# Kernel tuning notes

Hardware: AMD Instinct MI355X
Metric: run time of the kernel (lower is better)

The kernel has to match this reference:

```python
import jax, jax.numpy as jnp
import numpy as np
import math

B, S, H, N = 64, 512, 768, 16
C_COMP, C_REL = 5, 3
P = N * (N - 1)
LN_EPS = 1e-5

# ordered pair indices (i, j), i != j, row-major like the torch double loop
_PAIR_I, _PAIR_J = np.nonzero(~np.eye(N, dtype=bool))
_PAIR_I = jnp.asarray(_PAIR_I)
_PAIR_J = jnp.asarray(_PAIR_J)


def setup_inputs() -> dict:
    key = jax.random.key(0)
    ks = jax.random.split(key, 20)
    sc = 0.02
    p = lambda k, shape: (jax.random.normal(k, shape, jnp.float32) * sc)
    return {
        "last_hidden_state": jax.random.normal(ks[0], (B, S, H), jnp.float32),
        "span_starts": jax.random.randint(ks[1], (B, N), 0, 480).astype(jnp.int32),
        "span_lengths": jax.random.randint(ks[2], (B, N), 0, 31).astype(jnp.int32),
        "components": jax.random.randint(ks[3], (B, N), 0, C_COMP).astype(jnp.int32),
        "relations": jax.random.randint(ks[4], (B, P), 0, C_REL).astype(jnp.int32),
        # comp_classifier: Linear(H,512) -> Tanh -> Linear(512,C_COMP)
        "comp_w1": p(ks[5], (H, 512)), "comp_b1": jnp.zeros((512,), jnp.float32),
        "comp_w2": p(ks[6], (512, C_COMP)), "comp_b2": jnp.zeros((C_COMP,), jnp.float32),
        # Attention(H, H), no bias
        "wq": p(ks[7], (H, H)), "wk": p(ks[8], (H, H)), "wv": p(ks[9], (H, H)),
        # LayerNorm(H)
        "ln_g": jnp.ones((H,), jnp.float32), "ln_b": jnp.zeros((H,), jnp.float32),
        # rel_classifier: Linear(2H,512) -> Tanh -> Linear(512,C_REL)
        "rel_w1": p(ks[10], (2 * H, 512)), "rel_b1": jnp.zeros((512,), jnp.float32),
        "rel_w2": p(ks[11], (512, C_REL)), "rel_b2": jnp.zeros((C_REL,), jnp.float32),
    }


def _ce_mean(logits, gold):
    # logits [M, C], gold [M] -> scalar mean cross entropy
    logp = jax.nn.log_softmax(logits, axis=-1)
    return -jnp.mean(jnp.take_along_axis(logp, gold[:, None].astype(jnp.int32), axis=-1))


def reference(last_hidden_state, span_starts, span_lengths, components, relations,
              comp_w1, comp_b1, comp_w2, comp_b2,
              wq, wk, wv, ln_g, ln_b,
              rel_w1, rel_b1, rel_w2, rel_b2):
    # --- per-span mean pooling (inclusive end = start + length), masked+vectorized ---
    pos = jnp.arange(S)
    ends = span_starts + span_lengths
    mask = ((pos[None, None, :] >= span_starts[:, :, None]) &
            (pos[None, None, :] <= ends[:, :, None])).astype(jnp.float32)  # [B,N,S]
    lens = (span_lengths + 1).astype(jnp.float32)
    pooled = jnp.einsum('bns,bsh->bnh', mask, last_hidden_state) / lens[:, :, None]  # [B,N,H]
    # dropout(p=0.2) is identity in eval mode

    # --- component classifier ---
    comp_logits = jnp.tanh(pooled @ comp_w1 + comp_b1) @ comp_w2 + comp_b2  # [B,N,C_COMP]

    # --- small self-attention over spans ---
    q = pooled @ wq; k = pooled @ wk; v = pooled @ wv
    scores = jax.nn.softmax(jnp.einsum('bnd,bmd->bnm', q, k) / math.sqrt(H), axis=-1)
    attn = jnp.einsum('bnm,bmh->bnh', scores, v)

    # --- residual + layernorm ---
    x = pooled + attn
    mu = jnp.mean(x, axis=-1, keepdims=True)
    var = jnp.mean((x - mu) ** 2, axis=-1, keepdims=True)
    x = (x - mu) * jax.lax.rsqrt(var + LN_EPS) * ln_g + ln_b  # [B,N,H]

    # --- O(N^2) pairwise relation classification (ordered pairs i != j) ---
    pair_feat = jnp.concatenate([x[:, _PAIR_I, :], x[:, _PAIR_J, :]], axis=-1)  # [B,P,2H]
    rel_logits = jnp.tanh(pair_feat @ rel_w1 + rel_b1) @ rel_w2 + rel_b2  # [B,P,C_REL]

    loss_comp = _ce_mean(comp_logits.reshape(-1, C_COMP), components.reshape(-1))
    loss_rel = _ce_mean(rel_logits.reshape(-1, C_REL), relations.reshape(-1))
    return (comp_logits.reshape(-1, C_COMP), rel_logits.reshape(-1, C_REL), loss_comp, loss_rel)
```

## Files before the change

kernel.cpp:

```cpp
#include <hip/hip_runtime.h>

#define BB 64
#define SS 512
#define HH 768
#define NSPAN 16
#define PP 240
#define CCOMP 5
#define CREL 3

typedef unsigned short u16;
typedef __attribute__((ext_vector_type(8))) short bf16x8;
typedef __attribute__((ext_vector_type(4))) float f32x4;

__device__ __forceinline__ u16 f2bf(float f) {
    union { float f; unsigned int i; } v; v.f = f;
    unsigned int x = v.i;
    unsigned int lsb = (x >> 16) & 1u;
    x += 0x7fffu + lsb;
    return (u16)(x >> 16);
}

__device__ __forceinline__ float ftanh(float x) {
    float xc = fminf(fmaxf(x, -15.f), 15.f);
    float e = __expf(2.f * xc);
    return (e - 1.f) / (e + 1.f);
}

__global__ __launch_bounds__(256) void prep_pool_kernel(
    const float* __restrict__ cw1, const float* __restrict__ wq,
    const float* __restrict__ wk, const float* __restrict__ wv,
    const float* __restrict__ rw1, u16* __restrict__ wcat_t, u16* __restrict__ relw_t,
    const float* __restrict__ lhs, const int* __restrict__ starts,
    const int* __restrict__ lens, float* __restrict__ pooled, u16* __restrict__ pooled_bf) {
    __shared__ u16 Ls[32][36];
    int tid = threadIdx.x;
    if (blockIdx.x < 2880) {
        int blk = blockIdx.x;
        const float* W; int ldw, nt; u16* outp;
        if (blk < 384)        {             W = cw1; ldw = 512; nt = 16; outp = wcat_t; }
        else if (blk < 960)   { blk -= 384; W = wq;  ldw = 768; nt = 24; outp = wcat_t + (size_t)512 * 768; }
        else if (blk < 1536)  { blk -= 960; W = wk;  ldw = 768; nt = 24; outp = wcat_t + (size_t)1280 * 768; }
        else if (blk < 2112)  { blk -= 1536; W = wv; ldw = 768; nt = 24; outp = wcat_t + (size_t)2048 * 768; }
        else if (blk < 2496)  { blk -= 2112; W = rw1; ldw = 512; nt = 16; outp = relw_t; }
        else                  { blk -= 2496; W = rw1 + (size_t)768 * 512; ldw = 512; nt = 16; outp = relw_t + (size_t)512 * 768; }
        int tk = blk / nt, tn = blk % nt;
        int k0 = tk * 32, n0 = tn * 32;
        int tx = tid & 31, ty = tid >> 5;
#pragma unroll
        for (int r = 0; r < 4; ++r) {
            int k = ty + r * 8;
            Ls[tx][k] = f2bf(W[(size_t)(k0 + k) * ldw + n0 + tx]);
        }
        __syncthreads();
#pragma unroll
        for (int r = 0; r < 4; ++r) {
            int n = ty + r * 8;
            outp[(size_t)(n0 + n) * 768 + k0 + tx] = Ls[n][tx];
        }
    } else {
        int bn = blockIdx.x - 2880;
        int b = bn >> 4;
        int st = starts[bn];
        int ln = lens[bn];
        const float* base = lhs + ((size_t)b * SS + st) * HH;
        float a0 = 0.f, a1 = 0.f, a2 = 0.f;
        for (int s = 0; s <= ln; ++s) {
            const float* row = base + (size_t)s * HH;
            a0 += row[tid];
            a1 += row[tid + 256];
            a2 += row[tid + 512];
        }
        float inv = 1.0f / (float)(ln + 1);
        a0 *= inv; a1 *= inv; a2 *= inv;
        float* out = pooled + (size_t)bn * HH;
        u16* outb = pooled_bf + (size_t)bn * HH;
        out[tid] = a0;       out[tid + 256] = a1;       out[tid + 512] = a2;
        outb[tid] = f2bf(a0); outb[tid + 256] = f2bf(a1); outb[tid + 512] = f2bf(a2);
    }
}

__global__ __launch_bounds__(256) void gemm_pw_kernel(
    const u16* __restrict__ pooled_bf, const u16* __restrict__ wcat_t,
    const float* __restrict__ comp_b1, float* __restrict__ y2) {
    __shared__ u16 As[128][72];
    __shared__ u16 Bs[64][72];
    int ccol0 = blockIdx.x * 64;
    int row0 = blockIdx.y * 128;
    int act = (ccol0 < 512);
    int tid = threadIdx.x;
    int lane = tid & 63, w = tid >> 6;
    int q = lane >> 4, l15 = lane & 15;
    int wm = w * 32;
    int r = tid >> 2, c0 = (tid & 3) * 16;
    const u16* ga = pooled_bf + (size_t)(row0 + r) * 768 + c0;
    const u16* gb = wcat_t + (size_t)(ccol0 + r) * 768 + c0;
    const u16* ga2 = ga + (size_t)64 * 768;
    f32x4 acc[2][4];
#pragma unroll
    for (int i = 0; i < 2; ++i)
#pragma unroll
        for (int j = 0; j < 4; ++j) acc[i][j] = (f32x4){0.f, 0.f, 0.f, 0.f};

    uint4 va00 = *(const uint4*)(ga);
    uint4 va01 = *(const uint4*)(ga + 8);
    uint4 va10 = *(const uint4*)(ga2);
    uint4 va11 = *(const uint4*)(ga2 + 8);
    uint4 vb0 = *(const uint4*)(gb);
    uint4 vb1 = *(const uint4*)(gb + 8);
    for (int k0 = 0; k0 < 768; k0 += 64) {
        __syncthreads();
        *(uint4*)(&As[r][c0]) = va00;
        *(uint4*)(&As[r][c0 + 8]) = va01;
        *(uint4*)(&As[r + 64][c0]) = va10;
        *(uint4*)(&As[r + 64][c0 + 8]) = va11;
        *(uint4*)(&Bs[r][c0]) = vb0;
        *(uint4*)(&Bs[r][c0 + 8]) = vb1;
        __syncthreads();
        if (k0 + 64 < 768) {
            va00 = *(const uint4*)(ga + k0 + 64);
            va01 = *(const uint4*)(ga + k0 + 72);
            va10 = *(const uint4*)(ga2 + k0 + 64);
            va11 = *(const uint4*)(ga2 + k0 + 72);
            vb0 = *(const uint4*)(gb + k0 + 64);
            vb1 = *(const uint4*)(gb + k0 + 72);
        }
#pragma unroll
        for (int ks = 0; ks < 2; ++ks) {
            bf16x8 a0 = *(const bf16x8*)(&As[wm + l15][ks * 32 + q * 8]);
            bf16x8 a1 = *(const bf16x8*)(&As[wm + 16 + l15][ks * 32 + q * 8]);
#pragma unroll
            for (int tn = 0; tn < 4; ++tn) {
                bf16x8 bt = *(const bf16x8*)(&Bs[tn * 16 + l15][ks * 32 + q * 8]);
                acc[0][tn] = __builtin_amdgcn_mfma_f32_16x16x32_bf16(a0, bt, acc[0][tn], 0, 0, 0);
                acc[1][tn] = __builtin_amdgcn_mfma_f32_16x16x32_bf16(a1, bt, acc[1][tn], 0, 0, 0);
            }
        }
    }
#pragma unroll
    for (int tm = 0; tm < 2; ++tm)
#pragma unroll
        for (int tn = 0; tn < 4; ++tn)
#pragma unroll
            for (int reg = 0; reg < 4; ++reg) {
                int rr = row0 + wm + tm * 16 + q * 4 + reg;
                int cc = ccol0 + tn * 16 + l15;
                float v = acc[tm][tn][reg];
                if (act) v = ftanh(v + comp_b1[cc]);
                y2[(size_t)rr * 2816 + cc] = v;
            }
}

__global__ __launch_bounds__(256) void gemm_z_kernel(
    const u16* __restrict__ x_bf, const u16* __restrict__ relw_t, float* __restrict__ Z) {
    __shared__ u16 As[32][72];
    __shared__ u16 Bs[64][72];
    int ccol0 = blockIdx.x * 64;
    int row0 = blockIdx.y * 32;
    int tid = threadIdx.x;
    int lane = tid & 63, w = tid >> 6;
    int q = lane >> 4, l15 = lane & 15;
    int wm = (w & 1) * 16, wn = (w >> 1) * 32;
    int ra = tid >> 3, ca = (tid & 7) * 8;
    int rb = tid >> 2, cb = (tid & 3) * 16;
    const u16* ga = x_bf + (size_t)(row0 + ra) * 768 + ca;
    const u16* gb = relw_t + (size_t)(ccol0 + rb) * 768 + cb;
    f32x4 acc[2];
    acc[0] = (f32x4){0.f, 0.f, 0.f, 0.f};
    acc[1] = (f32x4){0.f, 0.f, 0.f, 0.f};

    uint4 va = *(const uint4*)(ga);
    uint4 vb0 = *(const uint4*)(gb);
    uint4 vb1 = *(const uint4*)(gb + 8);
    for (int k0 = 0; k0 < 768; k0 += 64) {
        __syncthreads();
        *(uint4*)(&As[ra][ca]) = va;
        *(uint4*)(&Bs[rb][cb]) = vb0;
        *(uint4*)(&Bs[rb][cb + 8]) = vb1;
        __syncthreads();
        if (k0 + 64 < 768) {
            va = *(const uint4*)(ga + k0 + 64);
            vb0 = *(const uint4*)(gb + k0 + 64);
            vb1 = *(const uint4*)(gb + k0 + 72);
        }
#pragma unroll
        for (int ks = 0; ks < 2; ++ks) {
            bf16x8 a0 = *(const bf16x8*)(&As[wm + l15][ks * 32 + q * 8]);
            bf16x8 b0 = *(const bf16x8*)(&Bs[wn + l15][ks * 32 + q * 8]);
            bf16x8 b1 = *(const bf16x8*)(&Bs[wn + 16 + l15][ks * 32 + q * 8]);
            acc[0] = __builtin_amdgcn_mfma_f32_16x16x32_bf16(a0, b0, acc[0], 0, 0, 0);
            acc[1] = __builtin_amdgcn_mfma_f32_16x16x32_bf16(a0, b1, acc[1], 0, 0, 0);
        }
    }
#pragma unroll
    for (int tn = 0; tn < 2; ++tn)
#pragma unroll
        for (int reg = 0; reg < 4; ++reg) {
            int rr = row0 + wm + q * 4 + reg;
            int cc = ccol0 + wn + tn * 16 + l15;
            Z[(size_t)rr * 1024 + cc] = acc[tn][reg];
        }
}

__global__ __launch_bounds__(256) void attn_ln_kernel(
    const float* __restrict__ y2, const float* __restrict__ pooled,
    const float* __restrict__ ln_g, const float* __restrict__ ln_b,
    u16* __restrict__ x_bf) {
    __shared__ float ks[16][772];
    __shared__ float Ssm[16][17];
    int b = blockIdx.x;
    int tid = threadIdx.x;
    int n = tid >> 4;
    int hl = tid & 15;

    for (int u = 0; u < 48; ++u) {
        int h = hl + (u << 4);
        ks[n][h] = y2[((size_t)(b * 16 + n)) * 2816 + 1280 + h];
    }
    __syncthreads();

    int m = tid & 15;
    const float* qrow = y2 + ((size_t)(b * 16 + n)) * 2816 + 512;
    float dot = 0.f;
    for (int h = 0; h < 768; h += 4) {
        float4 qv = *(const float4*)(qrow + h);
        float4 kv = *(const float4*)(&ks[m][h]);
        dot += qv.x * kv.x + qv.y * kv.y + qv.z * kv.z + qv.w * kv.w;
    }
    float sval = dot * 0.03608439182435161f;
    float mx = sval;
#pragma unroll
    for (int off = 8; off >= 1; off >>= 1) mx = fmaxf(mx, __shfl_xor(mx, off, 16));
    float pexp = __expf(sval - mx);
    float psum = pexp;
#pragma unroll
    for (int off = 8; off >= 1; off >>= 1) psum += __shfl_xor(psum, off, 16);
    Ssm[n][m] = pexp / psum;
    __syncthreads();

    for (int u = 0; u < 48; ++u) {
        int h = hl + (u << 4);
        ks[n][h] = y2[((size_t)(b * 16 + n)) * 2816 + 2048 + h];
    }
    __syncthreads();

    float sc[16];
#pragma unroll
    for (int mm = 0; mm < 16; ++mm) sc[mm] = Ssm[n][mm];
    int row = b * 16 + n;
    const float* prow = pooled + (size_t)row * HH;
    float xv[48];
    float ssum = 0.f, ssq = 0.f;
    for (int u = 0; u < 48; ++u) {
        int h = hl + (u << 4);
        float a = 0.f;
#pragma unroll
        for (int mm = 0; mm < 16; ++mm) a += sc[mm] * ks[mm][h];
        float v = prow[h] + a;
        xv[u] = v;
        ssum += v;
        ssq += v * v;
    }
#pragma unroll
    for (int off = 8; off >= 1; off >>= 1) {
        ssum += __shfl_xor(ssum, off, 16);
        ssq += __shfl_xor(ssq, off, 16);
    }
    float mu = ssum * (1.0f / 768.0f);
    float var = ssq * (1.0f / 768.0f) - mu * mu;
    float rs = rsqrtf(var + 1e-5f);
    u16* xrow_bf = x_bf + (size_t)row * HH;
    for (int u = 0; u < 48; ++u) {
        int h = hl + (u << 4);
        xrow_bf[h] = f2bf((xv[u] - mu) * rs * ln_g[h] + ln_b[h]);
    }
}

__global__ __launch_bounds__(256) void heads_kernel(
    const float* __restrict__ Z, const float* __restrict__ rb1,
    const float* __restrict__ rw2, const float* __restrict__ rb2,
    const int* __restrict__ rels,
    const float* __restrict__ y2, const float* __restrict__ cw2,
    const float* __restrict__ cb2, const int* __restrict__ comps,
    float* __restrict__ out, float* __restrict__ rel_p, float* __restrict__ comp_p) {
    __shared__ float Zs[16][1024];
    __shared__ float rw2s[1536];
    __shared__ float rb1s[512];
    __shared__ float red[4];
    int tid = threadIdx.x;
    int wave = tid >> 6, lane = tid & 63;
    if (blockIdx.x < 256) {
        int b = blockIdx.x >> 2;
        int quarter = blockIdx.x & 3;
        const float* zb = Z + (size_t)(b * 16) * 1024;
#pragma unroll
        for (int u = 0; u < 16; ++u) {
            *(float4*)(&Zs[u][tid * 4]) = *(const float4*)(zb + (size_t)u * 1024 + tid * 4);
        }
#pragma unroll
        for (int u = 0; u < 6; ++u) rw2s[tid + u * 256] = rw2[tid + u * 256];
        rb1s[tid] = rb1[tid];
        rb1s[tid + 256] = rb1[tid + 256];
        __syncthreads();

        float lsum = 0.f;
        for (int it = 0; it < 15; ++it) {
            int p = quarter * 60 + wave * 15 + it;
            int i = p / 15;
            int jj = p - i * 15;
            int j = jj + (jj >= i ? 1 : 0);
            float a0 = 0.f, a1 = 0.f, a2 = 0.f;
#pragma unroll
            for (int t = 0; t < 8; ++t) {
                int c = lane + (t << 6);
                float h = ftanh(Zs[i][c] + Zs[j][512 + c] + rb1s[c]);
                a0 += h * rw2s[c * 3 + 0];
                a1 += h * rw2s[c * 3 + 1];
                a2 += h * rw2s[c * 3 + 2];
            }
#pragma unroll
            for (int off = 32; off >= 1; off >>= 1) {
                a0 += __shfl_down(a0, off);
                a1 += __shfl_down(a1, off);
                a2 += __shfl_down(a2, off);
            }
            if (lane == 0) {
                int row = b * PP + p;
                float l0 = a0 + rb2[0];
                float l1 = a1 + rb2[1];
                float l2 = a2 + rb2[2];
                float mx = fmaxf(l0, fmaxf(l1, l2));
                float se = __expf(l0 - mx) + __expf(l1 - mx) + __expf(l2 - mx);
                float lse = __logf(se) + mx;
                int g = rels[row];
                float lg = (g == 0) ? l0 : ((g == 1) ? l1 : l2);
                lsum += lse - lg;
                float* o = out + 5120 + (size_t)row * 3;
                o[0] = l0; o[1] = l1; o[2] = l2;
            }
        }
        if (lane == 0) red[wave] = lsum;
        __syncthreads();
        if (tid == 0) rel_p[blockIdx.x] = red[0] + red[1] + red[2] + red[3];
    } else {
        int row = (blockIdx.x - 256) * 4 + wave;
        const float* hrow = y2 + (size_t)row * 2816;
        float acc[CCOMP] = {0.f, 0.f, 0.f, 0.f, 0.f};
#pragma unroll
        for (int t = 0; t < 8; ++t) {
            int c = lane + (t << 6);
            float h = hrow[c];
#pragma unroll
            for (int cc = 0; cc < CCOMP; ++cc) acc[cc] += h * cw2[c * CCOMP + cc];
        }
#pragma unroll
        for (int cc = 0; cc < CCOMP; ++cc)
#pragma unroll
            for (int off = 32; off >= 1; off >>= 1) acc[cc] += __shfl_down(acc[cc], off);
        if (lane == 0) {
            float l[CCOMP];
            float mx = -1e30f;
#pragma unroll
            for (int cc = 0; cc < CCOMP; ++cc) { l[cc] = acc[cc] + cb2[cc]; mx = fmaxf(mx, l[cc]); }
            float se = 0.f;
#pragma unroll
            for (int cc = 0; cc < CCOMP; ++cc) se += __expf(l[cc] - mx);
            float lse = __logf(se) + mx;
            red[wave] = lse - l[comps[row]];
#pragma unroll
            for (int cc = 0; cc < CCOMP; ++cc) out[row * CCOMP + cc] = l[cc];
        }
        __syncthreads();
        if (tid == 0) comp_p[blockIdx.x - 256] = red[0] + red[1] + red[2] + red[3];
    }
}

__global__ __launch_bounds__(256) void finalize_kernel(
    const float* __restrict__ comp_p, const float* __restrict__ rel_p,
    float* __restrict__ out) {
    __shared__ float rc[4], rr[4];
    int tid = threadIdx.x;
    int wave = tid >> 6, lane = tid & 63;
    float sc = comp_p[tid];
    float sr = rel_p[tid];
#pragma unroll
    for (int off = 32; off >= 1; off >>= 1) {
        sc += __shfl_down(sc, off);
        sr += __shfl_down(sr, off);
    }
    if (lane == 0) { rc[wave] = sc; rr[wave] = sr; }
    __syncthreads();
    if (tid == 0) {
        out[51200] = (rc[0] + rc[1] + rc[2] + rc[3]) * (1.0f / 1024.0f);
        out[51201] = (rr[0] + rr[1] + rr[2] + rr[3]) * (1.0f / 15360.0f);
    }
}

extern "C" void kernel_launch(void* const* d_in, const int* in_sizes, int n_in,
                              void* d_out, int out_size, void* d_ws, size_t ws_size,
                              hipStream_t stream) {
    const float* lhs     = (const float*)d_in[0];
    const int* starts    = (const int*)d_in[1];
    const int* lens      = (const int*)d_in[2];
    const int* comps     = (const int*)d_in[3];
    const int* rels      = (const int*)d_in[4];
    const float* comp_w1 = (const float*)d_in[5];
    const float* comp_b1 = (const float*)d_in[6];
    const float* comp_w2 = (const float*)d_in[7];
    const float* comp_b2 = (const float*)d_in[8];
    const float* wq      = (const float*)d_in[9];
    const float* wk      = (const float*)d_in[10];
    const float* wv      = (const float*)d_in[11];
    const float* ln_g    = (const float*)d_in[12];
    const float* ln_b    = (const float*)d_in[13];
    const float* rel_w1  = (const float*)d_in[14];
    const float* rel_b1  = (const float*)d_in[15];
    const float* rel_w2  = (const float*)d_in[16];
    const float* rel_b2  = (const float*)d_in[17];
    float* out = (float*)d_out;
    float* ws = (float*)d_ws;

    float* pooled = ws;
    float* y2     = pooled + 786432;
    float* Z      = y2 + 2883584;
    float* comp_p = Z + 1048576;
    float* rel_p  = comp_p + 256;
    u16* pooled_bf = (u16*)(rel_p + 256);
    u16* x_bf      = pooled_bf + 786432;
    u16* wcat_t    = x_bf + 786432;
    u16* relw_t    = wcat_t + 2162688;

    prep_pool_kernel<<<3904, 256, 0, stream>>>(comp_w1, wq, wk, wv, rel_w1, wcat_t, relw_t,
                                               lhs, starts, lens, pooled, pooled_bf);
    gemm_pw_kernel<<<dim3(44, 8), 256, 0, stream>>>(pooled_bf, wcat_t, comp_b1, y2);
    attn_ln_kernel<<<64, 256, 0, stream>>>(y2, pooled, ln_g, ln_b, x_bf);
    gemm_z_kernel<<<dim3(16, 32), 256, 0, stream>>>(x_bf, relw_t, Z);
    heads_kernel<<<512, 256, 0, stream>>>(Z, rel_b1, rel_w2, rel_b2, rels,
                                          y2, comp_w2, comp_b2, comps,
                                          out, rel_p, comp_p);
    finalize_kernel<<<1, 256, 0, stream>>>(comp_p, rel_p, out);
}
```

Baseline: 248.4 us.

## Fuse pipeline into single cooperative persistent kernel with grid syncs

Replaces six separate kernel launches with one cooperative kernel of 256 persistent blocks that loop over each stage's work units and use grid-wide syncs between stages. It keeps a multi-launch fallback selected by a phase argument if cooperative launch fails. The relation-head stage now stores Z in shared memory as bf16 instead of fp32. The intent is to remove launch gaps and inter-kernel drain, at the cost of lower per-stage parallelism, reduced occupancy from the large shared buffer, and grid-sync overhead.

```diff
diff --git a/kernel.cpp b/kernel.cpp
--- a/kernel.cpp
+++ b/kernel.cpp
@@ -1,9 +1,11 @@
 #include <hip/hip_runtime.h>
+#include <hip/hip_cooperative_groups.h>
+
+namespace cg = cooperative_groups;
 
 #define BB 64
 #define SS 512
 #define HH 768
-#define NSPAN 16
 #define PP 240
 #define CCOMP 5
 #define CREL 3
@@ -19,292 +21,333 @@
     x += 0x7fffu + lsb;
     return (u16)(x >> 16);
 }
-
+__device__ __forceinline__ float bf2f(u16 u) {
+    union { unsigned int i; float f; } v; v.i = ((unsigned int)u) << 16; return v.f;
+}
 __device__ __forceinline__ float ftanh(float x) {
     float xc = fminf(fmaxf(x, -15.f), 15.f);
     float e = __expf(2.f * xc);
     return (e - 1.f) / (e + 1.f);
 }
 
-__global__ __launch_bounds__(256) void prep_pool_kernel(
-    const float* __restrict__ cw1, const float* __restrict__ wq,
-    const float* __restrict__ wk, const float* __restrict__ wv,
-    const float* __restrict__ rw1, u16* __restrict__ wcat_t, u16* __restrict__ relw_t,
-    const float* __restrict__ lhs, const int* __restrict__ starts,
-    const int* __restrict__ lens, float* __restrict__ pooled, u16* __restrict__ pooled_bf) {
-    __shared__ u16 Ls[32][36];
-    int tid = threadIdx.x;
-    if (blockIdx.x < 2880) {
-        int blk = blockIdx.x;
-        const float* W; int ldw, nt; u16* outp;
-        if (blk < 384)        {             W = cw1; ldw = 512; nt = 16; outp = wcat_t; }
-        else if (blk < 960)   { blk -= 384; W = wq;  ldw = 768; nt = 24; outp = wcat_t + (size_t)512 * 768; }
-        else if (blk < 1536)  { blk -= 960; W = wk;  ldw = 768; nt = 24; outp = wcat_t + (size_t)1280 * 768; }
-        else if (blk < 2112)  { blk -= 1536; W = wv; ldw = 768; nt = 24; outp = wcat_t + (size_t)2048 * 768; }
-        else if (blk < 2496)  { blk -= 2112; W = rw1; ldw = 512; nt = 16; outp = relw_t; }
-        else                  { blk -= 2496; W = rw1 + (size_t)768 * 512; ldw = 512; nt = 16; outp = relw_t + (size_t)512 * 768; }
-        int tk = blk / nt, tn = blk % nt;
-        int k0 = tk * 32, n0 = tn * 32;
-        int tx = tid & 31, ty = tid >> 5;
-#pragma unroll
-        for (int r = 0; r < 4; ++r) {
-            int k = ty + r * 8;
-            Ls[tx][k] = f2bf(W[(size_t)(k0 + k) * ldw + n0 + tx]);
-        }
+__global__ __launch_bounds__(256) void fused_kernel(
+    const float* __restrict__ lhs, const int* __restrict__ starts, const int* __restrict__ lens,
+    const int* __restrict__ comps, const int* __restrict__ rels,
+    const float* __restrict__ cw1, const float* __restrict__ cb1,
+    const float* __restrict__ cw2, const float* __restrict__ cb2,
+    const float* __restrict__ wq, const float* __restrict__ wk, const float* __restrict__ wv,
+    const float* __restrict__ ln_g, const float* __restrict__ ln_b,
+    const float* __restrict__ rw1, const float* __restrict__ rb1,
+    const float* __restrict__ rw2, const float* __restrict__ rb2,
+    float* __restrict__ out, float* __restrict__ pooled, float* __restrict__ y2,
+    float* __restrict__ Z, float* __restrict__ comp_p, float* __restrict__ rel_p,
+    u16* __restrict__ pooled_bf, u16* __restrict__ x_bf,
+    u16* __restrict__ wcat_t, u16* __restrict__ relw_t, int phase) {
+    __shared__ __align__(16) char smem[50560];
+    const int tid = threadIdx.x;
+    const int blk = blockIdx.x;
+    const int gsz = (int)gridDim.x;
+    const int lane = tid & 63;
+    const int wid = tid >> 6;
+
+    if (phase == 0 || phase == 1) {
+        u16 (*Ls)[36] = (u16(*)[36])smem;
+        for (int u = blk; u < 3904; u += gsz) {
+            if (u < 2880) {
+                int b2 = u;
+                const float* W; int ldw, nt; u16* outp;
+                if (b2 < 384)        {             W = cw1; ldw = 512; nt = 16; outp = wcat_t; }
+                else if (b2 < 960)   { b2 -= 384;  W = wq;  ldw = 768; nt = 24; outp = wcat_t + (size_t)512 * 768; }
+                else if (b2 < 1536)  { b2 -= 960;  W = wk;  ldw = 768; nt = 24; outp = wcat_t + (size_t)1280 * 768; }
+                else if (b2 < 2112)  { b2 -= 1536; W = wv;  ldw = 768; nt = 24; outp = wcat_t + (size_t)2048 * 768; }
+                else if (b2 < 2496)  { b2 -= 2112; W = rw1; ldw = 512; nt = 16; outp = relw_t; }
+                else                 { b2 -= 2496; W = rw1 + (size_t)768 * 512; ldw = 512; nt = 16; outp = relw_t + (size_t)512 * 768; }
+                int tk = b2 / nt, tn = b2 % nt;
+                int k0 = tk * 32, n0 = tn * 32;
+                int tx = tid & 31, ty = tid >> 5;
+                __syncthreads();
+#pragma unroll
+                for (int r = 0; r < 4; ++r) {
+                    int k = ty + r * 8;
+                    Ls[tx][k] = f2bf(W[(size_t)(k0 + k) * ldw + n0 + tx]);
+                }
+                __syncthreads();
+#pragma unroll
+                for (int r = 0; r < 4; ++r) {
+                    int n = ty + r * 8;
+                    outp[(size_t)(n0 + n) * 768 + k0 + tx] = Ls[n][tx];
+                }
+            } else {
+                int bn = u - 2880;
+                int b = bn >> 4;
+                int st = starts[bn];
+                int ln = lens[bn];
+                const float* base = lhs + ((size_t)b * SS + st) * HH;
+                float a0 = 0.f, a1 = 0.f, a2 = 0.f;
+                for (int s = 0; s <= ln; ++s) {
+                    const float* row = base + (size_t)s * HH;
+                    a0 += row[tid];
+                    a1 += row[tid + 256];
+                    a2 += row[tid + 512];
+                }
+                float inv = 1.0f / (float)(ln + 1);
+                a0 *= inv; a1 *= inv; a2 *= inv;
+                float* o = pooled + (size_t)bn * HH;
+                u16* ob = pooled_bf + (size_t)bn * HH;
+                o[tid] = a0;        o[tid + 256] = a1;        o[tid + 512] = a2;
+                ob[tid] = f2bf(a0); ob[tid + 256] = f2bf(a1); ob[tid + 512] = f2bf(a2);
+            }
+        }
+    }
+    if (phase == 0) cg::this_grid().sync();
+
+    if (phase == 0 || phase == 2) {
+        u16 (*As)[72] = (u16(*)[72])smem;
+        u16 (*Bs)[72] = (u16(*)[72])(smem + 18432);
+        for (int t = blk; t < 352; t += gsz) {
+            int ccol0 = (t % 44) * 64;
+            int row0 = (t / 44) * 128;
+            int act = (ccol0 < 512);
+            int q = lane >> 4, l15 = lane & 15;
+            int wm = wid * 32;
+            int r = tid >> 2, c0 = (tid & 3) * 16;
+            const u16* ga = pooled_bf + (size_t)(row0 + r) * 768 + c0;
+            const u16* gb = wcat_t + (size_t)(ccol0 + r) * 768 + c0;
+            const u16* ga2 = ga + (size_t)64 * 768;
+            f32x4 acc[2][4];
+#pragma unroll
+            for (int i = 0; i < 2; ++i)
+#pragma unroll
+                for (int j = 0; j < 4; ++j) acc[i][j] = (f32x4){0.f, 0.f, 0.f, 0.f};
+
+            uint4 va00 = *(const uint4*)(ga);
+            uint4 va01 = *(const uint4*)(ga + 8);
+            uint4 va10 = *(const uint4*)(ga2);
+            uint4 va11 = *(const uint4*)(ga2 + 8);
+            uint4 vb0 = *(const uint4*)(gb);
+            uint4 vb1 = *(const uint4*)(gb + 8);
+            for (int k0 = 0; k0 < 768; k0 += 64) {
+                __syncthreads();
+                *(uint4*)(&As[r][c0]) = va00;
+                *(uint4*)(&As[r][c0 + 8]) = va01;
+                *(uint4*)(&As[r + 64][c0]) = va10;
+                *(uint4*)(&As[r + 64][c0 + 8]) = va11;
+                *(uint4*)(&Bs[r][c0]) = vb0;
+                *(uint4*)(&Bs[r][c0 + 8]) = vb1;
+                __syncthreads();
+                if (k0 + 64 < 768) {
+                    va00 = *(const uint4*)(ga + k0 + 64);
+                    va01 = *(const uint4*)(ga + k0 + 72);
+                    va10 = *(const uint4*)(ga2 + k0 + 64);
+                    va11 = *(const uint4*)(ga2 + k0 + 72);
+                    vb0 = *(const uint4*)(gb + k0 + 64);
+                    vb1 = *(const uint4*)(gb + k0 + 72);
+                }
+#pragma unroll
+                for (int ks = 0; ks < 2; ++ks) {
+                    bf16x8 a0 = *(const bf16x8*)(&As[wm + l15][ks * 32 + q * 8]);
+                    bf16x8 a1 = *(const bf16x8*)(&As[wm + 16 + l15][ks * 32 + q * 8]);
+#pragma unroll
+                    for (int tn = 0; tn < 4; ++tn) {
+                        bf16x8 bt = *(const bf16x8*)(&Bs[tn * 16 + l15][ks * 32 + q * 8]);
+                        acc[0][tn] = __builtin_amdgcn_mfma_f32_16x16x32_bf16(a0, bt, acc[0][tn], 0, 0, 0);
+                        acc[1][tn] = __builtin_amdgcn_mfma_f32_16x16x32_bf16(a1, bt, acc[1][tn], 0, 0, 0);
+                    }
+                }
+            }
+#pragma unroll
+            for (int tm = 0; tm < 2; ++tm)
+#pragma unroll
+                for (int tn = 0; tn < 4; ++tn)
+#pragma unroll
+                    for (int reg = 0; reg < 4; ++reg) {
+                        int rr = row0 + wm + tm * 16 + q * 4 + reg;
+                        int cc = ccol0 + tn * 16 + l15;
+                        float v = acc[tm][tn][reg];
+                        if (act) v = ftanh(v + cb1[cc]);
+                        y2[(size_t)rr * 2816 + cc] = v;
+                    }
+        }
+    }
+    if (phase == 0) cg::this_grid().sync();
+
+    if (phase == 0 || phase == 3) {
+        for (int u = blk; u < 320; u += gsz) {
+            __syncthreads();
+            if (u < 64) {
+                float (*ks)[772] = (float(*)[772])smem;
+                float (*Ssm)[17] = (float(*)[17])(smem + 49408);
+                int b = u;
+                int n = tid >> 4;
+                int hl = tid & 15;
+                for (int v = 0; v < 48; ++v) {
+                    int h = hl + (v << 4);
+                    ks[n][h] = y2[((size_t)(b * 16 + n)) * 2816 + 1280 + h];
+                }
+                __syncthreads();
+                int m = tid & 15;
+                const float* qrow = y2 + ((size_t)(b * 16 + n)) * 2816 + 512;
+                float dot = 0.f;
+                for (int h = 0; h < 768; h += 4) {
+                    float4 qv = *(const float4*)(qrow + h);
+                    float4 kv = *(const float4*)(&ks[m][h]);
+                    dot += qv.x * kv.x + qv.y * kv.y + qv.z * kv.z + qv.w * kv.w;
+                }
+                float sval = dot * 0.03608439182435161f;
+                float mx = sval;
+#pragma unroll
+                for (int off = 8; off >= 1; off >>= 1) mx = fmaxf(mx, __shfl_xor(mx, off, 16));
+                float pexp = __expf(sval - mx);
+                float psum = pexp;
+#pragma unroll
+                for (int off = 8; off >= 1; off >>= 1) psum += __shfl_xor(psum, off, 16);
+                Ssm[n][m] = pexp / psum;
+                __syncthreads();
+                for (int v = 0; v < 48; ++v) {
+                    int h = hl + (v << 4);
+                    ks[n][h] = y2[((size_t)(b * 16 + n)) * 2816 + 2048 + h];
+                }
+                __syncthreads();
+                float sc[16];
+#pragma unroll
+                for (int mm = 0; mm < 16; ++mm) sc[mm] = Ssm[n][mm];
+                int row = b * 16 + n;
+                const float* prow = pooled + (size_t)row * HH;
+                float xv[48];
+                float ssum = 0.f, ssq = 0.f;
+                for (int v = 0; v < 48; ++v) {
+                    int h = hl + (v << 4);
+                    float a = 0.f;
+#pragma unroll
+                    for (int mm = 0; mm < 16; ++mm) a += sc[mm] * ks[mm][h];
+                    float vv = prow[h] + a;
+                    xv[v] = vv;
+                    ssum += vv;
+                    ssq += vv * vv;
+                }
+#pragma unroll
+                for (int off = 8; off >= 1; off >>= 1) {
+                    ssum += __shfl_xor(ssum, off, 16);
+                    ssq += __shfl_xor(ssq, off, 16);
+                }
+                float mu = ssum * (1.0f / 768.0f);
+                float var = ssq * (1.0f / 768.0f) - mu * mu;
+                float rs = rsqrtf(var + 1e-5f);
+                u16* xrow_bf = x_bf + (size_t)row * HH;
+                for (int v = 0; v < 48; ++v) {
+                    int h = hl + (v << 4);
+                    xrow_bf[h] = f2bf((xv[v] - mu) * rs * ln_g[h] + ln_b[h]);
+                }
+            } else {
+                float* red = (float*)smem;
+                int row = (u - 64) * 4 + wid;
+                const float* hrow = y2 + (size_t)row * 2816;
+                float acc[CCOMP] = {0.f, 0.f, 0.f, 0.f, 0.f};
+#pragma unroll
+                for (int t = 0; t < 8; ++t) {
+                    int c = lane + (t << 6);
+                    float h = hrow[c];
+#pragma unroll
+                    for (int cc = 0; cc < CCOMP; ++cc) acc[cc] += h * cw2[c * CCOMP + cc];
+                }
+#pragma unroll
+                for (int cc = 0; cc < CCOMP; ++cc)
+#pragma unroll
+                    for (int off = 32; off >= 1; off >>= 1) acc[cc] += __shfl_down(acc[cc], off);
+                if (lane == 0) {
+                    float l[CCOMP];
+                    float mx = -1e30f;
+#pragma unroll
+                    for (int cc = 0; cc < CCOMP; ++cc) { l[cc] = acc[cc] + cb2[cc]; mx = fmaxf(mx, l[cc]); }
+                    float se = 0.f;
+#pragma unroll
+                    for (int cc = 0; cc < CCOMP; ++cc) se += __expf(l[cc] - mx);
+                    float lse = __logf(se) + mx;
+                    red[wid] = lse - l[comps[row]];
+#pragma unroll
+                    for (int cc = 0; cc < CCOMP; ++cc) out[row * CCOMP + cc] = l[cc];
+                }
+                __syncthreads();
+                if (tid == 0) comp_p[u - 64] = red[0] + red[1] + red[2] + red[3];
+            }
+        }
+    }
+    if (phase == 0) cg::this_grid().sync();
+
+    if (phase == 0 || phase == 4) {
+        u16 (*As2)[72] = (u16(*)[72])smem;
+        u16 (*Bs2)[72] = (u16(*)[72])(smem + 4608);
+        for (int t = blk; t < 512; t += gsz) {
+            int ccol0 = (t & 15) * 64;
+            int row0 = (t >> 4) * 32;
+            int q = lane >> 4, l15 = lane & 15;
+            int wm = (wid & 1) * 16, wn = (wid >> 1) * 32;
+            int ra = tid >> 3, ca = (tid & 7) * 8;
+            int rb = tid >> 2, cb = (tid & 3) * 16;
+            const u16* ga = x_bf + (size_t)(row0 + ra) * 768 + ca;
+            const u16* gb = relw_t + (size_t)(ccol0 + rb) * 768 + cb;
+            f32x4 acc2[2];
+            acc2[0] = (f32x4){0.f, 0.f, 0.f, 0.f};
+            acc2[1] = (f32x4){0.f, 0.f, 0.f, 0.f};
+            uint4 va = *(const uint4*)(ga);
+            uint4 vb0 = *(const uint4*)(gb);
+            uint4 vb1 = *(const uint4*)(gb + 8);
+            for (int k0 = 0; k0 < 768; k0 += 64) {
+                __syncthreads();
+                *(uint4*)(&As2[ra][ca]) = va;
+                *(uint4*)(&Bs2[rb][cb]) = vb0;
+                *(uint4*)(&Bs2[rb][cb + 8]) = vb1;
+                __syncthreads();
+                if (k0 + 64 < 768) {
+                    va = *(const uint4*)(ga + k0 + 64);
+                    vb0 = *(const uint4*)(gb + k0 + 64);
+                    vb1 = *(const uint4*)(gb + k0 + 72);
+                }
+#pragma unroll
+                for (int ks2 = 0; ks2 < 2; ++ks2) {
+                    bf16x8 a0 = *(const bf16x8*)(&As2[wm + l15][ks2 * 32 + q * 8]);
+                    bf16x8 b0 = *(const bf16x8*)(&Bs2[wn + l15][ks2 * 32 + q * 8]);
+                    bf16x8 b1 = *(const bf16x8*)(&Bs2[wn + 16 + l15][ks2 * 32 + q * 8]);
+                    acc2[0] = __builtin_amdgcn_mfma_f32_16x16x32_bf16(a0, b0, acc2[0], 0, 0, 0);
+                    acc2[1] = __builtin_amdgcn_mfma_f32_16x16x32_bf16(a0, b1, acc2[1], 0, 0, 0);
+                }
+            }
+#pragma unroll
+            for (int tn = 0; tn < 2; ++tn)
+#pragma unroll
+                for (int reg = 0; reg < 4; ++reg) {
+                    int rr = row0 + wm + q * 4 + reg;
+                    int cc = ccol0 + wn + tn * 16 + l15;
+                    Z[(size_t)rr * 1024 + cc] = acc2[tn][reg];
+                }
+        }
+    }
+    if (phase == 0) cg::this_grid().sync();
+
+    if ((phase == 0 || phase == 5) && blk < 256) {
+        u16 (*Zs)[1024] = (u16(*)[1024])smem;
+        float* rw2s = (float*)(smem + 32768);
+        float* rb1s = (float*)(smem + 38912);
+        float* redr = (float*)(smem + 40960);
+        int b = blk >> 2;
+        int quarter = blk & 3;
+        const float* zb = Z + (size_t)(b * 16) * 1024;
         __syncthreads();
 #pragma unroll
-        for (int r = 0; r < 4; ++r) {
-            int n = ty + r * 8;
-            outp[(size_t)(n0 + n) * 768 + k0 + tx] = Ls[n][tx];
-        }
-    } else {
-        int bn = blockIdx.x - 2880;
-        int b = bn >> 4;
-        int st = starts[bn];
-        int ln = lens[bn];
-        const float* base = lhs + ((size_t)b * SS + st) * HH;
-        float a0 = 0.f, a1 = 0.f, a2 = 0.f;
-        for (int s = 0; s <= ln; ++s) {
-            const float* row = base + (size_t)s * HH;
-            a0 += row[tid];
-            a1 += row[tid + 256];
-            a2 += row[tid + 512];
-        }
-        float inv = 1.0f / (float)(ln + 1);
-        a0 *= inv; a1 *= inv; a2 *= inv;
-        float* out = pooled + (size_t)bn * HH;
-        u16* outb = pooled_bf + (size_t)bn * HH;
-        out[tid] = a0;       out[tid + 256] = a1;       out[tid + 512] = a2;
-        outb[tid] = f2bf(a0); outb[tid + 256] = f2bf(a1); outb[tid + 512] = f2bf(a2);
-    }
-}
-
-__global__ __launch_bounds__(256) void gemm_pw_kernel(
-    const u16* __restrict__ pooled_bf, const u16* __restrict__ wcat_t,
-    const float* __restrict__ comp_b1, float* __restrict__ y2) {
-    __shared__ u16 As[128][72];
-    __shared__ u16 Bs[64][72];
-    int ccol0 = blockIdx.x * 64;
-    int row0 = blockIdx.y * 128;
-    int act = (ccol0 < 512);
-    int tid = threadIdx.x;
-    int lane = tid & 63, w = tid >> 6;
-    int q = lane >> 4, l15 = lane & 15;
-    int wm = w * 32;
-    int r = tid >> 2, c0 = (tid & 3) * 16;
-    const u16* ga = pooled_bf + (size_t)(row0 + r) * 768 + c0;
-    const u16* gb = wcat_t + (size_t)(ccol0 + r) * 768 + c0;
-    const u16* ga2 = ga + (size_t)64 * 768;
-    f32x4 acc[2][4];
-#pragma unroll
-    for (int i = 0; i < 2; ++i)
-#pragma unroll
-        for (int j = 0; j < 4; ++j) acc[i][j] = (f32x4){0.f, 0.f, 0.f, 0.f};
-
-    uint4 va00 = *(const uint4*)(ga);
-    uint4 va01 = *(const uint4*)(ga + 8);
-    uint4 va10 = *(const uint4*)(ga2);
-    uint4 va11 = *(const uint4*)(ga2 + 8);
-    uint4 vb0 = *(const uint4*)(gb);
-    uint4 vb1 = *(const uint4*)(gb + 8);
-    for (int k0 = 0; k0 < 768; k0 += 64) {
-        __syncthreads();
-        *(uint4*)(&As[r][c0]) = va00;
-        *(uint4*)(&As[r][c0 + 8]) = va01;
-        *(uint4*)(&As[r + 64][c0]) = va10;
-        *(uint4*)(&As[r + 64][c0 + 8]) = va11;
-        *(uint4*)(&Bs[r][c0]) = vb0;
-        *(uint4*)(&Bs[r][c0 + 8]) = vb1;
-        __syncthreads();
-        if (k0 + 64 < 768) {
-            va00 = *(const uint4*)(ga + k0 + 64);
-            va01 = *(const uint4*)(ga + k0 + 72);
-            va10 = *(const uint4*)(ga2 + k0 + 64);
-            va11 = *(const uint4*)(ga2 + k0 + 72);
-            vb0 = *(const uint4*)(gb + k0 + 64);
-            vb1 = *(const uint4*)(gb + k0 + 72);
-        }
-#pragma unroll
-        for (int ks = 0; ks < 2; ++ks) {
-            bf16x8 a0 = *(const bf16x8*)(&As[wm + l15][ks * 32 + q * 8]);
-            bf16x8 a1 = *(const bf16x8*)(&As[wm + 16 + l15][ks * 32 + q * 8]);
-#pragma unroll
-            for (int tn = 0; tn < 4; ++tn) {
-                bf16x8 bt = *(const bf16x8*)(&Bs[tn * 16 + l15][ks * 32 + q * 8]);
-                acc[0][tn] = __builtin_amdgcn_mfma_f32_16x16x32_bf16(a0, bt, acc[0][tn], 0, 0, 0);
-                acc[1][tn] = __builtin_amdgcn_mfma_f32_16x16x32_bf16(a1, bt, acc[1][tn], 0, 0, 0);
-            }
-        }
-    }
-#pragma unroll
-    for (int tm = 0; tm < 2; ++tm)
-#pragma unroll
-        for (int tn = 0; tn < 4; ++tn)
-#pragma unroll
-            for (int reg = 0; reg < 4; ++reg) {
-                int rr = row0 + wm + tm * 16 + q * 4 + reg;
-                int cc = ccol0 + tn * 16 + l15;
-                float v = acc[tm][tn][reg];
-                if (act) v = ftanh(v + comp_b1[cc]);
-                y2[(size_t)rr * 2816 + cc] = v;
-            }
-}
-
-__global__ __launch_bounds__(256) void gemm_z_kernel(
-    const u16* __restrict__ x_bf, const u16* __restrict__ relw_t, float* __restrict__ Z) {
-    __shared__ u16 As[32][72];
-    __shared__ u16 Bs[64][72];
-    int ccol0 = blockIdx.x * 64;
-    int row0 = blockIdx.y * 32;
-    int tid = threadIdx.x;
-    int lane = tid & 63, w = tid >> 6;
-    int q = lane >> 4, l15 = lane & 15;
-    int wm = (w & 1) * 16, wn = (w >> 1) * 32;
-    int ra = tid >> 3, ca = (tid & 7) * 8;
-    int rb = tid >> 2, cb = (tid & 3) * 16;
-    const u16* ga = x_bf + (size_t)(row0 + ra) * 768 + ca;
-    const u16* gb = relw_t + (size_t)(ccol0 + rb) * 768 + cb;
-    f32x4 acc[2];
-    acc[0] = (f32x4){0.f, 0.f, 0.f, 0.f};
-    acc[1] = (f32x4){0.f, 0.f, 0.f, 0.f};
-
-    uint4 va = *(const uint4*)(ga);
-    uint4 vb0 = *(const uint4*)(gb);
-    uint4 vb1 = *(const uint4*)(gb + 8);
-    for (int k0 = 0; k0 < 768; k0 += 64) {
-        __syncthreads();
-        *(uint4*)(&As[ra][ca]) = va;
-        *(uint4*)(&Bs[rb][cb]) = vb0;
-        *(uint4*)(&Bs[rb][cb + 8]) = vb1;
-        __syncthreads();
-        if (k0 + 64 < 768) {
-            va = *(const uint4*)(ga + k0 + 64);
-            vb0 = *(const uint4*)(gb + k0 + 64);
-            vb1 = *(const uint4*)(gb + k0 + 72);
-        }
-#pragma unroll
-        for (int ks = 0; ks < 2; ++ks) {
-            bf16x8 a0 = *(const bf16x8*)(&As[wm + l15][ks * 32 + q * 8]);
-            bf16x8 b0 = *(const bf16x8*)(&Bs[wn + l15][ks * 32 + q * 8]);
-            bf16x8 b1 = *(const bf16x8*)(&Bs[wn + 16 + l15][ks * 32 + q * 8]);
-            acc[0] = __builtin_amdgcn_mfma_f32_16x16x32_bf16(a0, b0, acc[0], 0, 0, 0);
-            acc[1] = __builtin_amdgcn_mfma_f32_16x16x32_bf16(a0, b1, acc[1], 0, 0, 0);
-        }
-    }
-#pragma unroll
-    for (int tn = 0; tn < 2; ++tn)
-#pragma unroll
-        for (int reg = 0; reg < 4; ++reg) {
-            int rr = row0 + wm + q * 4 + reg;
-            int cc = ccol0 + wn + tn * 16 + l15;
-            Z[(size_t)rr * 1024 + cc] = acc[tn][reg];
-        }
-}
-
-__global__ __launch_bounds__(256) void attn_ln_kernel(
-    const float* __restrict__ y2, const float* __restrict__ pooled,
-    const float* __restrict__ ln_g, const float* __restrict__ ln_b,
-    u16* __restrict__ x_bf) {
-    __shared__ float ks[16][772];
-    __shared__ float Ssm[16][17];
-    int b = blockIdx.x;
-    int tid = threadIdx.x;
-    int n = tid >> 4;
-    int hl = tid & 15;
-
-    for (int u = 0; u < 48; ++u) {
-        int h = hl + (u << 4);
-        ks[n][h] = y2[((size_t)(b * 16 + n)) * 2816 + 1280 + h];
-    }
-    __syncthreads();
-
-    int m = tid & 15;
-    const float* qrow = y2 + ((size_t)(b * 16 + n)) * 2816 + 512;
-    float dot = 0.f;
-    for (int h = 0; h < 768; h += 4) {
-        float4 qv = *(const float4*)(qrow + h);
-        float4 kv = *(const float4*)(&ks[m][h]);
-        dot += qv.x * kv.x + qv.y * kv.y + qv.z * kv.z + qv.w * kv.w;
-    }
-    float sval = dot * 0.03608439182435161f;
-    float mx = sval;
-#pragma unroll
-    for (int off = 8; off >= 1; off >>= 1) mx = fmaxf(mx, __shfl_xor(mx, off, 16));
-    float pexp = __expf(sval - mx);
-    float psum = pexp;
-#pragma unroll
-    for (int off = 8; off >= 1; off >>= 1) psum += __shfl_xor(psum, off, 16);
-    Ssm[n][m] = pexp / psum;
-    __syncthreads();
-
-    for (int u = 0; u < 48; ++u) {
-        int h = hl + (u << 4);
-        ks[n][h] = y2[((size_t)(b * 16 + n)) * 2816 + 2048 + h];
-    }
-    __syncthreads();
-
-    float sc[16];
-#pragma unroll
-    for (int mm = 0; mm < 16; ++mm) sc[mm] = Ssm[n][mm];
-    int row = b * 16 + n;
-    const float* prow = pooled + (size_t)row * HH;
-    float xv[48];
-    float ssum = 0.f, ssq = 0.f;
-    for (int u = 0; u < 48; ++u) {
-        int h = hl + (u << 4);
-        float a = 0.f;
-#pragma unroll
-        for (int mm = 0; mm < 16; ++mm) a += sc[mm] * ks[mm][h];
-        float v = prow[h] + a;
-        xv[u] = v;
-        ssum += v;
-        ssq += v * v;
-    }
-#pragma unroll
-    for (int off = 8; off >= 1; off >>= 1) {
-        ssum += __shfl_xor(ssum, off, 16);
-        ssq += __shfl_xor(ssq, off, 16);
-    }
-    float mu = ssum * (1.0f / 768.0f);
-    float var = ssq * (1.0f / 768.0f) - mu * mu;
-    float rs = rsqrtf(var + 1e-5f);
-    u16* xrow_bf = x_bf + (size_t)row * HH;
-    for (int u = 0; u < 48; ++u) {
-        int h = hl + (u << 4);
-        xrow_bf[h] = f2bf((xv[u] - mu) * rs * ln_g[h] + ln_b[h]);
-    }
-}
-
-__global__ __launch_bounds__(256) void heads_kernel(
-    const float* __restrict__ Z, const float* __restrict__ rb1,
-    const float* __restrict__ rw2, const float* __restrict__ rb2,
-    const int* __restrict__ rels,
-    const float* __restrict__ y2, const float* __restrict__ cw2,
-    const float* __restrict__ cb2, const int* __restrict__ comps,
-    float* __restrict__ out, float* __restrict__ rel_p, float* __restrict__ comp_p) {
-    __shared__ float Zs[16][1024];
-    __shared__ float rw2s[1536];
-    __shared__ float rb1s[512];
-    __shared__ float red[4];
-    int tid = threadIdx.x;
-    int wave = tid >> 6, lane = tid & 63;
-    if (blockIdx.x < 256) {
-        int b = blockIdx.x >> 2;
-        int quarter = blockIdx.x & 3;
-        const float* zb = Z + (size_t)(b * 16) * 1024;
-#pragma unroll
         for (int u = 0; u < 16; ++u) {
-            *(float4*)(&Zs[u][tid * 4]) = *(const float4*)(zb + (size_t)u * 1024 + tid * 4);
+            float4 v = *(const float4*)(zb + (size_t)u * 1024 + tid * 4);
+            ushort4 pk;
+            pk.x = f2bf(v.x); pk.y = f2bf(v.y); pk.z = f2bf(v.z); pk.w = f2bf(v.w);
+            *(ushort4*)(&Zs[u][tid * 4]) = pk;
         }
 #pragma unroll
         for (int u = 0; u < 6; ++u) rw2s[tid + u * 256] = rw2[tid + u * 256];
         rb1s[tid] = rb1[tid];
         rb1s[tid + 256] = rb1[tid + 256];
         __syncthreads();
-
         float lsum = 0.f;
         for (int it = 0; it < 15; ++it) {
-            int p = quarter * 60 + wave * 15 + it;
+            int p = quarter * 60 + wid * 15 + it;
             int i = p / 15;
             int jj = p - i * 15;
             int j = jj + (jj >= i ? 1 : 0);
@@ -312,7 +355,7 @@
 #pragma unroll
             for (int t = 0; t < 8; ++t) {
                 int c = lane + (t << 6);
-                float h = ftanh(Zs[i][c] + Zs[j][512 + c] + rb1s[c]);
+                float h = ftanh(bf2f(Zs[i][c]) + bf2f(Zs[j][512 + c]) + rb1s[c]);
                 a0 += h * rw2s[c * 3 + 0];
                 a1 += h * rw2s[c * 3 + 1];
                 a2 += h * rw2s[c * 3 + 2];
@@ -338,60 +381,29 @@
                 o[0] = l0; o[1] = l1; o[2] = l2;
             }
         }
-        if (lane == 0) red[wave] = lsum;
+        if (lane == 0) redr[wid] = lsum;
         __syncthreads();
-        if (tid == 0) rel_p[blockIdx.x] = red[0] + red[1] + red[2] + red[3];
-    } else {
-        int row = (blockIdx.x - 256) * 4 + wave;
-        const float* hrow = y2 + (size_t)row * 2816;
-        float acc[CCOMP] = {0.f, 0.f, 0.f, 0.f, 0.f};
-#pragma unroll
-        for (int t = 0; t < 8; ++t) {
-            int c = lane + (t << 6);
-            float h = hrow[c];
-#pragma unroll
-            for (int cc = 0; cc < CCOMP; ++cc) acc[cc] += h * cw2[c * CCOMP + cc];
-        }
-#pragma unroll
-        for (int cc = 0; cc < CCOMP; ++cc)
-#pragma unroll
-            for (int off = 32; off >= 1; off >>= 1) acc[cc] += __shfl_down(acc[cc], off);
-        if (lane == 0) {
-            float l[CCOMP];
-            float mx = -1e30f;
-#pragma unroll
-            for (int cc = 0; cc < CCOMP; ++cc) { l[cc] = acc[cc] + cb2[cc]; mx = fmaxf(mx, l[cc]); }
-            float se = 0.f;
-#pragma unroll
-            for (int cc = 0; cc < CCOMP; ++cc) se += __expf(l[cc] - mx);
-            float lse = __logf(se) + mx;
-            red[wave] = lse - l[comps[row]];
-#pragma unroll
-            for (int cc = 0; cc < CCOMP; ++cc) out[row * CCOMP + cc] = l[cc];
-        }
+        if (tid == 0) rel_p[blk] = redr[0] + redr[1] + redr[2] + redr[3];
+    }
+    if (phase == 0) cg::this_grid().sync();
+
+    if ((phase == 0 || phase == 6) && blk == 0) {
         __syncthreads();
-        if (tid == 0) comp_p[blockIdx.x - 256] = red[0] + red[1] + red[2] + red[3];
-    }
-}
-
-__global__ __launch_bounds__(256) void finalize_kernel(
-    const float* __restrict__ comp_p, const float* __restrict__ rel_p,
-    float* __restrict__ out) {
-    __shared__ float rc[4], rr[4];
-    int tid = threadIdx.x;
-    int wave = tid >> 6, lane = tid & 63;
-    float sc = comp_p[tid];
-    float sr = rel_p[tid];
-#pragma unroll
-    for (int off = 32; off >= 1; off >>= 1) {
-        sc += __shfl_down(sc, off);
-        sr += __shfl_down(sr, off);
-    }
-    if (lane == 0) { rc[wave] = sc; rr[wave] = sr; }
-    __syncthreads();
-    if (tid == 0) {
-        out[51200] = (rc[0] + rc[1] + rc[2] + rc[3]) * (1.0f / 1024.0f);
-        out[51201] = (rr[0] + rr[1] + rr[2] + rr[3]) * (1.0f / 15360.0f);
+        float* rc = (float*)smem;
+        float* rr = (float*)(smem + 16);
+        float sc = comp_p[tid];
+        float sr = rel_p[tid];
+#pragma unroll
+        for (int off = 32; off >= 1; off >>= 1) {
+            sc += __shfl_down(sc, off);
+            sr += __shfl_down(sr, off);
+        }
+        if (lane == 0) { rc[wid] = sc; rr[wid] = sr; }
+        __syncthreads();
+        if (tid == 0) {
+            out[51200] = (rc[0] + rc[1] + rc[2] + rc[3]) * (1.0f / 1024.0f);
+            out[51201] = (rr[0] + rr[1] + rr[2] + rr[3]) * (1.0f / 15360.0f);
+        }
     }
 }
 
@@ -429,13 +441,44 @@
     u16* wcat_t    = x_bf + 786432;
     u16* relw_t    = wcat_t + 2162688;
 
-    prep_pool_kernel<<<3904, 256, 0, stream>>>(comp_w1, wq, wk, wv, rel_w1, wcat_t, relw_t,
-                                               lhs, starts, lens, pooled, pooled_bf);
-    gemm_pw_kernel<<<dim3(44, 8), 256, 0, stream>>>(pooled_bf, wcat_t, comp_b1, y2);
-    attn_ln_kernel<<<64, 256, 0, stream>>>(y2, pooled, ln_g, ln_b, x_bf);
-    gemm_z_kernel<<<dim3(16, 32), 256, 0, stream>>>(x_bf, relw_t, Z);
-    heads_kernel<<<512, 256, 0, stream>>>(Z, rel_b1, rel_w2, rel_b2, rels,
-                                          y2, comp_w2, comp_b2, comps,
-                                          out, rel_p, comp_p);
-    finalize_kernel<<<1, 256, 0, stream>>>(comp_p, rel_p, out);
+    int phase0 = 0;
+    void* args[] = {
+        (void*)&lhs, (void*)&starts, (void*)&lens, (void*)&comps, (void*)&rels,
+        (void*)&comp_w1, (void*)&comp_b1, (void*)&comp_w2, (void*)&comp_b2,
+        (void*)&wq, (void*)&wk, (void*)&wv, (void*)&ln_g, (void*)&ln_b,
+        (void*)&rel_w1, (void*)&rel_b1, (void*)&rel_w2, (void*)&rel_b2,
+        (void*)&out, (void*)&pooled, (void*)&y2, (void*)&Z,
+        (void*)&comp_p, (void*)&rel_p,
+        (void*)&pooled_bf, (void*)&x_bf, (void*)&wcat_t, (void*)&relw_t,
+        (void*)&phase0
+    };
+    hipError_t err = hipLaunchCooperativeKernel((const void*)fused_kernel, dim3(256), dim3(256),
+                                                args, 0, stream);
+    if (err != hipSuccess) {
+        (void)hipGetLastError();
+        fused_kernel<<<3904, 256, 0, stream>>>(lhs, starts, lens, comps, rels,
+            comp_w1, comp_b1, comp_w2, comp_b2, wq, wk, wv, ln_g, ln_b,
+            rel_w1, rel_b1, rel_w2, rel_b2, out, pooled, y2, Z, comp_p, rel_p,
+            pooled_bf, x_bf, wcat_t, relw_t, 1);
+        fused_kernel<<<352, 256, 0, stream>>>(lhs, starts, lens, comps, rels,
+            comp_w1, comp_b1, comp_w2, comp_b2, wq, wk, wv, ln_g, ln_b,
+            rel_w1, rel_b1, rel_w2, rel_b2, out, pooled, y2, Z, comp_p, rel_p,
+            pooled_bf, x_bf, wcat_t, relw_t, 2);
+        fused_kernel<<<320, 256, 0, stream>>>(lhs, starts, lens, comps, rels,
+            comp_w1, comp_b1, comp_w2, comp_b2, wq, wk, wv, ln_g, ln_b,
+            rel_w1, rel_b1, rel_w2, rel_b2, out, pooled, y2, Z, comp_p, rel_p,
+            pooled_bf, x_bf, wcat_t, relw_t, 3);
+        fused_kernel<<<512, 256, 0, stream>>>(lhs, starts, lens, comps, rels,
+            comp_w1, comp_b1, comp_w2, comp_b2, wq, wk, wv, ln_g, ln_b,
+            rel_w1, rel_b1, rel_w2, rel_b2, out, pooled, y2, Z, comp_p, rel_p,
+            pooled_bf, x_bf, wcat_t, relw_t, 4);
+        fused_kernel<<<256, 256, 0, stream>>>(lhs, starts, lens, comps, rels,
+            comp_w1, comp_b1, comp_w2, comp_b2, wq, wk, wv, ln_g, ln_b,
+            rel_w1, rel_b1, rel_w2, rel_b2, out, pooled, y2, Z, comp_p, rel_p,
+            pooled_bf, x_bf, wcat_t, relw_t, 5);
+        fused_kernel<<<1, 256, 0, stream>>>(lhs, starts, lens, comps, rels,
+            comp_w1, comp_b1, comp_w2, comp_b2, wq, wk, wv, ln_g, ln_b,
+            rel_w1, rel_b1, rel_w2, rel_b2, out, pooled, y2, Z, comp_p, rel_p,
+            pooled_bf, x_bf, wcat_t, relw_t, 6);
+    }
 }
```

After: 469.6 us. 1.89x slower.
